# Optimization experiments

Hardware: AMD Instinct MI355X
Metric: run time of the kernel (lower is better)

## Reference

```python
import jax, jax.numpy as jnp
import numpy as np

IN_FEATURES = 4096
OUT_FEATURES = 4096


def setup_inputs() -> dict:
    key = jax.random.key(0)
    k_x, k_w, k_ws, k_b = jax.random.split(key, 4)
    x = jax.random.normal(k_x, (4, 2048, IN_FEATURES), dtype=jnp.float16)
    # int8 weight in [-127, 127]
    weight = jax.random.randint(k_w, (OUT_FEATURES, IN_FEATURES), -127, 128, dtype=jnp.int32).astype(jnp.int8)
    # realistic small per-output-channel dequant scales (as produced by from_float)
    weight_scales = (jax.random.uniform(k_ws, (OUT_FEATURES,), dtype=jnp.float32) * 0.02 + 0.001).astype(jnp.float16)
    bias = (jax.random.normal(k_b, (1, OUT_FEATURES), dtype=jnp.float32) * 0.01).astype(jnp.float16)
    return {"x": x, "weight": weight, "weight_scales": weight_scales, "bias": bias}


def reference(x, weight, weight_scales, bias):
    x_shape = x.shape
    xf = x.reshape(-1, x_shape[-1]).astype(jnp.float32)  # [T, in]
    # dynamic per-token min-max quantization: scale = max|x| / 127
    x_scale = jnp.max(jnp.abs(xf), axis=-1, keepdims=True) / 127.0  # [T, 1]
    q_x = jnp.clip(jnp.round(xf / x_scale), -128, 127).astype(jnp.int8)  # [T, in]
    # int8 GEMM accumulated in int32: q_y = q_x @ weight.T
    q_y = jnp.matmul(q_x.astype(jnp.int32), weight.T.astype(jnp.int32))  # [T, out]
    # dequant: per-channel weight scale * per-token activation scale
    y = q_y.astype(jnp.float32) * weight_scales.astype(jnp.float32)[None, :] * x_scale
    y = y.astype(jnp.float16).reshape(*x_shape[:-1], -1)
    y = y + bias  # fp16 bias add, broadcasts [1, out]
    return y
```

## Files before the change

### kernel.cpp

```cpp
#include <hip/hip_runtime.h>
#include <hip/hip_bf16.h>
#include <stdint.h>

typedef int v4i __attribute__((ext_vector_type(4)));
typedef float v4f __attribute__((ext_vector_type(4)));

#define T_TOKENS 8192
#define KDIM 4096
#define NDIM 4096

#define BM 256
#define BN 256
#define BKB 128

__global__ __launch_bounds__(256) void conv_w(const int* __restrict__ w32,
                                              int8_t* __restrict__ w8) {
    int idx = blockIdx.x * 256 + threadIdx.x;
    const v4i* src = (const v4i*)w32 + (size_t)idx * 4;
    v4i p;
#pragma unroll
    for (int q = 0; q < 4; ++q) {
        v4i s = src[q];
        p[q] = (s[0] & 255) | ((s[1] & 255) << 8) | ((s[2] & 255) << 16)
             | ((s[3] & 255) << 24);
    }
    ((v4i*)w8)[idx] = p;
}

__global__ __launch_bounds__(256) void quant_x(const float* __restrict__ x,
                                               int8_t* __restrict__ qx,
                                               float* __restrict__ xs) {
    int t = blockIdx.x;
    int tid = threadIdx.x;
    const v4f* xrow = (const v4f*)(x + (size_t)t * KDIM);

    v4f vals[4];
    float m = 0.f;
#pragma unroll
    for (int q = 0; q < 4; ++q) {
        v4f v = xrow[q * 256 + tid];
        vals[q] = v;
        m = fmaxf(m, fmaxf(fmaxf(fabsf(v[0]), fabsf(v[1])),
                           fmaxf(fabsf(v[2]), fabsf(v[3]))));
    }
#pragma unroll
    for (int off = 32; off > 0; off >>= 1)
        m = fmaxf(m, __shfl_xor(m, off));

    __shared__ float wmax[4];
    __shared__ float sh_scale;
    int wave = tid >> 6;
    if ((tid & 63) == 0) wmax[wave] = m;
    __syncthreads();
    if (tid == 0) {
        float mm = fmaxf(fmaxf(wmax[0], wmax[1]), fmaxf(wmax[2], wmax[3]));
        float sc = mm / 127.0f;
        sh_scale = sc;
        xs[t] = sc;
    }
    __syncthreads();
    float sc = sh_scale;

    unsigned int* qrow = (unsigned int*)(qx + (size_t)t * KDIM);
#pragma unroll
    for (int q = 0; q < 4; ++q) {
        unsigned int packed = 0;
#pragma unroll
        for (int j = 0; j < 4; ++j) {
            float fq = rintf(vals[q][j] / sc);
            fq = fminf(fmaxf(fq, -128.f), 127.f);
            int b = (int)fq;
            packed |= ((unsigned int)(unsigned char)(b & 0xff)) << (8 * j);
        }
        qrow[q * 256 + tid] = packed;
    }
}

__global__ __launch_bounds__(512, 2) void gemm_i8(
        const int8_t* __restrict__ A, const int8_t* __restrict__ B,
        const float* __restrict__ xs, const float* __restrict__ wscale,
        const float* __restrict__ bias, float* __restrict__ out) {
    __shared__ char lds[131072];

    const int tid  = threadIdx.x;
    const int lane = tid & 63;
    const int w    = tid >> 6;
    const int wr   = w >> 2;
    const int wc   = w & 3;
    const int lrow = lane & 15;
    const int kg   = lane >> 4;
    const int swz  = (kg ^ ((lrow >> 1) & 3)) << 4;

    int flat = blockIdx.x;
    int f2 = (flat & 7) * 64 + (flat >> 3);
    int bm = f2 >> 4, bn = f2 & 15;

    const int8_t* Ab = A + (size_t)bm * BM * KDIM;
    const int8_t* Bb = B + (size_t)bn * BN * KDIM;

    const int srow = (w << 5) + (lane >> 2);
    const int sg16 = (((lane & 3) ^ ((lane >> 3) & 3)) << 4);
    const size_t goff = (size_t)srow * KDIM + sg16;

#define STAGE(gp, kbyte, lbase)                                                  \
    do {                                                                         \
        const int8_t* g0 = (gp) + goff + (kbyte);                                \
        char* l0 = (lbase) + (w << 11);                                          \
        __builtin_amdgcn_global_load_lds(                                        \
            (const __attribute__((address_space(1))) void*)g0,                   \
            (__attribute__((address_space(3))) void*)l0, 16, 0, 0);              \
        __builtin_amdgcn_global_load_lds(                                        \
            (const __attribute__((address_space(1))) void*)(g0 + (size_t)16 * KDIM), \
            (__attribute__((address_space(3))) void*)(l0 + 1024), 16, 0, 0);     \
    } while (0)

    v4i acc[8][4] = {};

    STAGE(Ab, 0,  lds + 0);
    STAGE(Bb, 0,  lds + 32768);
    STAGE(Ab, 64, lds + 16384);
    STAGE(Bb, 64, lds + 49152);
    asm volatile("s_waitcnt vmcnt(0)" ::: "memory");
    __builtin_amdgcn_s_barrier();
    asm volatile("" ::: "memory");

    const int abase = wr * 128 + lrow;
    const int bbase = wc * 64 + lrow;

    for (int t = 0; t < KDIM / BKB; ++t) {
        char* cur = lds + ((t & 1) << 16);
        char* nxt = lds + (((t + 1) & 1) << 16);
        int   nk  = ((t + 1) & 31) * BKB;

#pragma unroll
        for (int ks = 0; ks < 2; ++ks) {
            STAGE(Ab, nk + ks * 64, nxt + ks * 16384);
            STAGE(Bb, nk + ks * 64, nxt + 32768 + ks * 16384);

            const char* ap = cur + ks * 16384;
            const char* bp = cur + 32768 + ks * 16384;
            v4i af[8], bf[4];
#pragma unroll
            for (int m = 0; m < 8; ++m)
                af[m] = *(const v4i*)(ap + (abase + m * 16) * 64 + swz);
#pragma unroll
            for (int n = 0; n < 4; ++n)
                bf[n] = *(const v4i*)(bp + (bbase + n * 16) * 64 + swz);

            __builtin_amdgcn_s_setprio(1);
#pragma unroll
            for (int m = 0; m < 8; ++m)
#pragma unroll
                for (int n = 0; n < 4; ++n)
                    acc[m][n] = __builtin_amdgcn_mfma_i32_16x16x64_i8(
                        af[m], bf[n], acc[m][n], 0, 0, 0);
            __builtin_amdgcn_s_setprio(0);

            asm volatile("s_waitcnt vmcnt(4)" ::: "memory");
            __builtin_amdgcn_s_barrier();
            asm volatile("" ::: "memory");
        }
    }

    int rowg0 = bm * BM + wr * 128;
    int colg0 = bn * BN + wc * 64;
    float xsv[8][4];
#pragma unroll
    for (int m = 0; m < 8; ++m)
#pragma unroll
        for (int j = 0; j < 4; ++j)
            xsv[m][j] = xs[rowg0 + m * 16 + kg * 4 + j];

#pragma unroll
    for (int n = 0; n < 4; ++n) {
        int col = colg0 + n * 16 + lrow;
        float wsc = wscale[col];
        float bs  = bias[col];
#pragma unroll
        for (int m = 0; m < 8; ++m) {
#pragma unroll
            for (int j = 0; j < 4; ++j) {
                int row = rowg0 + m * 16 + kg * 4 + j;
                float y = (float)acc[m][n][j] * wsc * xsv[m][j] + bs;
                out[(size_t)row * NDIM + col] = y;
            }
        }
    }
#undef STAGE
}

extern "C" void kernel_launch(void* const* d_in, const int* in_sizes, int n_in,
                              void* d_out, int out_size, void* d_ws, size_t ws_size,
                              hipStream_t stream) {
    const float* x    = (const float*)d_in[0];
    const int*   w32  = (const int*)d_in[1];
    const float* wsc  = (const float*)d_in[2];
    const float* bias = (const float*)d_in[3];
    float* out = (float*)d_out;

    int8_t* qx = (int8_t*)d_ws;
    int8_t* w8 = (int8_t*)d_ws + (size_t)T_TOKENS * KDIM;
    float*  xs = (float*)((int8_t*)d_ws + (size_t)T_TOKENS * KDIM + (size_t)NDIM * KDIM);

    hipLaunchKernelGGL(conv_w, dim3(NDIM * KDIM / 16 / 256), dim3(256), 0, stream, w32, w8);
    hipLaunchKernelGGL(quant_x, dim3(T_TOKENS), dim3(256), 0, stream, x, qx, xs);
    hipLaunchKernelGGL(gemm_i8, dim3((T_TOKENS / BM) * (NDIM / BN)), dim3(512), 0, stream,
                       qx, w8, xs, wsc, bias, out);
}
```

Before: 393.1 us.

## Issue full next-tile prefetch up front and merge two k-substeps per barrier

```diff
diff --git a/kernel.cpp b/kernel.cpp
--- a/kernel.cpp
+++ b/kernel.cpp
@@ -98,28 +98,27 @@
     const int8_t* Ab = A + (size_t)bm * BM * KDIM;
     const int8_t* Bb = B + (size_t)bn * BN * KDIM;
 
-    const int srow = (w << 5) + (lane >> 2);
     const int sg16 = (((lane & 3) ^ ((lane >> 3) & 3)) << 4);
-    const size_t goff = (size_t)srow * KDIM + sg16;
-
-#define STAGE(gp, kbyte, lbase)                                                  \
+
+#define STAGE_HALF(gp, kbyte, lhalf)                                             \
     do {                                                                         \
-        const int8_t* g0 = (gp) + goff + (kbyte);                                \
-        char* l0 = (lbase) + (w << 11);                                          \
-        __builtin_amdgcn_global_load_lds(                                        \
-            (const __attribute__((address_space(1))) void*)g0,                   \
-            (__attribute__((address_space(3))) void*)l0, 16, 0, 0);              \
-        __builtin_amdgcn_global_load_lds(                                        \
-            (const __attribute__((address_space(1))) void*)(g0 + (size_t)16 * KDIM), \
-            (__attribute__((address_space(3))) void*)(l0 + 1024), 16, 0, 0);     \
+        _Pragma("unroll")                                                        \
+        for (int r_ = 0; r_ < 2; ++r_) {                                         \
+            int row_ = r_ * 128 + (w << 4) + (lane >> 2);                        \
+            const int8_t* g_ = (gp) + (size_t)row_ * KDIM + (kbyte) + sg16;      \
+            char* l_ = (lhalf) + (size_t)(r_ * 128 + (w << 4)) * 64;             \
+            __builtin_amdgcn_global_load_lds(                                    \
+                (const __attribute__((address_space(1))) void*)g_,               \
+                (__attribute__((address_space(3))) void*)l_, 16, 0, 0);          \
+        }                                                                        \
     } while (0)
 
     v4i acc[8][4] = {};
 
-    STAGE(Ab, 0,  lds + 0);
-    STAGE(Bb, 0,  lds + 32768);
-    STAGE(Ab, 64, lds + 16384);
-    STAGE(Bb, 64, lds + 49152);
+    STAGE_HALF(Ab, 0,  lds + 0);
+    STAGE_HALF(Ab, 64, lds + 16384);
+    STAGE_HALF(Bb, 0,  lds + 32768);
+    STAGE_HALF(Bb, 64, lds + 49152);
     asm volatile("s_waitcnt vmcnt(0)" ::: "memory");
     __builtin_amdgcn_s_barrier();
     asm volatile("" ::: "memory");
@@ -132,34 +131,43 @@
         char* nxt = lds + (((t + 1) & 1) << 16);
         int   nk  = ((t + 1) & 31) * BKB;
 
-#pragma unroll
-        for (int ks = 0; ks < 2; ++ks) {
-            STAGE(Ab, nk + ks * 64, nxt + ks * 16384);
-            STAGE(Bb, nk + ks * 64, nxt + 32768 + ks * 16384);
-
-            const char* ap = cur + ks * 16384;
-            const char* bp = cur + 32768 + ks * 16384;
-            v4i af[8], bf[4];
-#pragma unroll
-            for (int m = 0; m < 8; ++m)
-                af[m] = *(const v4i*)(ap + (abase + m * 16) * 64 + swz);
+        STAGE_HALF(Ab, nk,      nxt + 0);
+        STAGE_HALF(Ab, nk + 64, nxt + 16384);
+        STAGE_HALF(Bb, nk,      nxt + 32768);
+        STAGE_HALF(Bb, nk + 64, nxt + 49152);
+
+        v4i f0a[8], f1a[8], f0b[4], f1b[4];
+#pragma unroll
+        for (int m = 0; m < 8; ++m)
+            f0a[m] = *(const v4i*)(cur + (abase + m * 16) * 64 + swz);
+#pragma unroll
+        for (int n = 0; n < 4; ++n)
+            f0b[n] = *(const v4i*)(cur + 32768 + (bbase + n * 16) * 64 + swz);
+#pragma unroll
+        for (int m = 0; m < 8; ++m)
+            f1a[m] = *(const v4i*)(cur + 16384 + (abase + m * 16) * 64 + swz);
+#pragma unroll
+        for (int n = 0; n < 4; ++n)
+            f1b[n] = *(const v4i*)(cur + 49152 + (bbase + n * 16) * 64 + swz);
+
+        __builtin_amdgcn_s_setprio(1);
+#pragma unroll
+        for (int m = 0; m < 8; ++m)
 #pragma unroll
             for (int n = 0; n < 4; ++n)
-                bf[n] = *(const v4i*)(bp + (bbase + n * 16) * 64 + swz);
-
-            __builtin_amdgcn_s_setprio(1);
-#pragma unroll
-            for (int m = 0; m < 8; ++m)
-#pragma unroll
-                for (int n = 0; n < 4; ++n)
-                    acc[m][n] = __builtin_amdgcn_mfma_i32_16x16x64_i8(
-                        af[m], bf[n], acc[m][n], 0, 0, 0);
-            __builtin_amdgcn_s_setprio(0);
-
-            asm volatile("s_waitcnt vmcnt(4)" ::: "memory");
-            __builtin_amdgcn_s_barrier();
-            asm volatile("" ::: "memory");
-        }
+                acc[m][n] = __builtin_amdgcn_mfma_i32_16x16x64_i8(
+                    f0a[m], f0b[n], acc[m][n], 0, 0, 0);
+#pragma unroll
+        for (int m = 0; m < 8; ++m)
+#pragma unroll
+            for (int n = 0; n < 4; ++n)
+                acc[m][n] = __builtin_amdgcn_mfma_i32_16x16x64_i8(
+                    f1a[m], f1b[n], acc[m][n], 0, 0, 0);
+        __builtin_amdgcn_s_setprio(0);
+
+        asm volatile("s_waitcnt vmcnt(0)" ::: "memory");
+        __builtin_amdgcn_s_barrier();
+        asm volatile("" ::: "memory");
     }
 
     int rowg0 = bm * BM + wr * 128;
@@ -186,7 +194,7 @@
             }
         }
     }
-#undef STAGE
+#undef STAGE_HALF
 }
 
 extern "C" void kernel_launch(void* const* d_in, const int* in_sizes, int n_in,
```

Result: no change. 396.0 us (+0.7%).
